# Kernel optimization log

Measured on AMD Instinct MI355X. Metric: run time of the kernel, lower is better.

The kernel has to match this reference:

```python
import jax, jax.numpy as jnp
import numpy as np

B, N, D, S, ITERS = 64, 4096, 256, 8, 3
EPS = 1e-5


def _ln(x, g, b):
    m = jnp.mean(x, axis=-1, keepdims=True)
    v = jnp.mean((x - m) ** 2, axis=-1, keepdims=True)
    return (x - m) * jax.lax.rsqrt(v + EPS) * g + b


def setup_inputs() -> dict:
    key = jax.random.key(0)
    ks = jax.random.split(key, 20)
    s = 1.0 / np.sqrt(D)
    inp = {
        'x': jax.random.normal(ks[0], (B, N, D), jnp.float32),
        'noise': jax.random.normal(ks[1], (B, S, D), jnp.float32),
        'slot_mu': jax.random.normal(ks[2], (1, 1, D), jnp.float32),
        'slot_sigma': jax.random.normal(ks[3], (1, 1, D), jnp.float32) * 0.1,
        'Wq': jax.random.uniform(ks[4], (D, D), jnp.float32, -s, s),
        'bq': jnp.zeros((D,), jnp.float32),
        'Wk': jax.random.uniform(ks[5], (D, D), jnp.float32, -s, s),
        'bk': jnp.zeros((D,), jnp.float32),
        'Wv': jax.random.uniform(ks[6], (D, D), jnp.float32, -s, s),
        'bv': jnp.zeros((D,), jnp.float32),
        'W_ih': jax.random.uniform(ks[7], (3 * D, D), jnp.float32, -s, s),
        'b_ih': jnp.zeros((3 * D,), jnp.float32),
        'W_hh': jax.random.uniform(ks[8], (3 * D, D), jnp.float32, -s, s),
        'b_hh': jnp.zeros((3 * D,), jnp.float32),
        'W1': jax.random.uniform(ks[9], (D, D), jnp.float32, -s, s),
        'b1': jnp.zeros((D,), jnp.float32),
        'W2': jax.random.uniform(ks[10], (D, D), jnp.float32, -s, s),
        'b2': jnp.zeros((D,), jnp.float32),
        'g_in': jnp.ones((D,), jnp.float32), 'be_in': jnp.zeros((D,), jnp.float32),
        'g_sl': jnp.ones((D,), jnp.float32), 'be_sl': jnp.zeros((D,), jnp.float32),
        'g_mlp': jnp.ones((D,), jnp.float32), 'be_mlp': jnp.zeros((D,), jnp.float32),
    }
    return inp


def reference(x, noise, slot_mu, slot_sigma, Wq, bq, Wk, bk, Wv, bv,
              W_ih, b_ih, W_hh, b_hh, W1, b1, W2, b2,
              g_in, be_in, g_sl, be_sl, g_mlp, be_mlp):
    # slot init: mu + exp(sigma) * noise, broadcast over (B, S, D)
    slots = slot_mu + jnp.exp(slot_sigma) * noise

    xn = _ln(x, g_in, be_in)
    k = jnp.einsum('bnd,ed->bne', xn, Wk) + bk
    v = jnp.einsum('bnd,ed->bne', xn, Wv) + bv

    for _ in range(ITERS):
        sn = _ln(slots, g_sl, be_sl)
        q = jnp.einsum('bsd,ed->bse', sn, Wq) + bq
        attn_logits = jnp.einsum('bsd,bnd->bsn', q, k)
        attn = jax.nn.softmax(attn_logits, axis=-1)  # softmax over inputs N (as in source)
        updates = jnp.einsum('bnd,bsn->bsd', v, attn)

        # GRUCell: input=updates, hidden=slots (flattened over B*S)
        u = updates.reshape(-1, D)
        h = slots.reshape(-1, D)
        gx = u @ W_ih.T + b_ih
        gh = h @ W_hh.T + b_hh
        xr, xz, xn_g = jnp.split(gx, 3, axis=-1)
        hr, hz, hn_g = jnp.split(gh, 3, axis=-1)
        r = jax.nn.sigmoid(xr + hr)
        z = jax.nn.sigmoid(xz + hz)
        n = jnp.tanh(xn_g + r * hn_g)
        h = (1.0 - z) * n + z * h
        slots = h.reshape(x.shape[0], -1, D)

        m = _ln(slots, g_mlp, be_mlp)
        slots = slots + jax.nn.relu(m @ W1.T + b1) @ W2.T + b2
    return slots
```

## Files before the change

kernel.cpp:

```cpp
#include <hip/hip_runtime.h>

#define B_ 64
#define N_ 4096
#define D_ 256
#define S_ 8
#define EPSL 1e-5f

typedef _Float16 f16x8 __attribute__((ext_vector_type(8)));
typedef _Float16 f16x4 __attribute__((ext_vector_type(4)));
typedef float f32x4 __attribute__((ext_vector_type(4)));

__device__ __forceinline__ void gload_lds16_nt(const void* g, void* l){
    __builtin_amdgcn_global_load_lds(
        (const __attribute__((address_space(1))) unsigned int*)g,
        (__attribute__((address_space(3))) unsigned int*)l, 16, 0, 2);
}

__global__ __launch_bounds__(256) void k_ln_x(const float* __restrict__ x,
        const float* __restrict__ g, const float* __restrict__ be,
        _Float16* __restrict__ xn) {
    int w = threadIdx.x >> 6, l = threadIdx.x & 63;
    long row = (long)blockIdx.x * 4 + w;
    float4 xv = *(const float4*)(x + row * D_ + l * 4);
    float s = xv.x + xv.y + xv.z + xv.w;
    float q = xv.x*xv.x + xv.y*xv.y + xv.z*xv.z + xv.w*xv.w;
    #pragma unroll
    for (int m = 1; m < 64; m <<= 1) { s += __shfl_xor(s, m); q += __shfl_xor(q, m); }
    float mean = s * (1.0f/D_);
    float var = q * (1.0f/D_) - mean*mean;
    float inv = rsqrtf(var + EPSL);
    float4 gv = *(const float4*)(g + l*4);
    float4 bv = *(const float4*)(be + l*4);
    f16x4 o;
    o[0] = (_Float16)((xv.x-mean)*inv*gv.x + bv.x);
    o[1] = (_Float16)((xv.y-mean)*inv*gv.y + bv.y);
    o[2] = (_Float16)((xv.z-mean)*inv*gv.z + bv.z);
    o[3] = (_Float16)((xv.w-mean)*inv*gv.w + bv.w);
    *(f16x4*)(xn + row * D_ + l*4) = o;
}

__global__ __launch_bounds__(256) void k_wprep(const float* __restrict__ Whh,
        const float* __restrict__ W1, const float* __restrict__ W2,
        _Float16* __restrict__ Whhf, _Float16* __restrict__ W1f,
        _Float16* __restrict__ W2f) {
    int r = blockIdx.x, t = threadIdx.x;
    const float* src; _Float16* dst; int row;
    if (r < 768){ src = Whh; dst = Whhf; row = r; }
    else if (r < 1024){ src = W1; dst = W1f; row = r - 768; }
    else { src = W2; dst = W2f; row = r - 1024; }
    float v = src[(long)(r < 768 ? r : (r < 1024 ? r-768 : r-1024))*256 + t];
    long di = (long)((((row>>4)*8 + (t>>5))*64 + ((t>>3)&3)*16 + (row&15)))*8 + (t&7);
    dst[di] = (_Float16)v;
}

__global__ __launch_bounds__(256) void k_wprep2(const float* __restrict__ Wih,
        const float* __restrict__ Wv, const float* __restrict__ Wq,
        const float* __restrict__ Wk, const float* __restrict__ bih,
        const float* __restrict__ bv, const float* __restrict__ bq,
        _Float16* __restrict__ Wcf, _Float16* __restrict__ Wqkf,
        float* __restrict__ bc, float* __restrict__ cq) {
    __shared__ float a[4][256];
    int r = blockIdx.x, t = threadIdx.x;
    int w = t>>6, l = t&63;
    bool isC = (r < 192);
    if (isC){
        #pragma unroll
        for (int k=0;k<4;k++) a[k][t] = Wih[(long)(r*4+k)*256 + t];
    } else {
        int dbase = (r-192)*4;
        #pragma unroll
        for (int k=0;k<4;k++) a[k][t] = Wk[(long)t*256 + dbase + k];
    }
    __syncthreads();
    float ac[4] = {0.f,0.f,0.f,0.f};
    const float* Bm = isC ? Wv : Wq;
    for (int e=0;e<256;e++){
        float bvv = Bm[(long)e*256 + t];
        ac[0] += a[0][e]*bvv; ac[1] += a[1][e]*bvv;
        ac[2] += a[2][e]*bvv; ac[3] += a[3][e]*bvv;
    }
    _Float16* dst = isC ? Wcf : Wqkf;
    int rb = isC ? r*4 : (r-192)*4;
    #pragma unroll
    for (int k=0;k<4;k++){
        int row = rb + k;
        long di = (long)((((row>>4)*8 + (t>>5))*64 + ((t>>3)&3)*16 + (row&15)))*8 + (t&7);
        dst[di] = (_Float16)ac[k];
    }
    if (w < 4){
        const float* bvec = isC ? bv : bq;
        float p = 0.f;
        #pragma unroll
        for (int q=0;q<4;q++) p += a[w][l + q*64] * bvec[l + q*64];
        #pragma unroll
        for (int m=1;m<64;m<<=1) p += __shfl_xor(p, m);
        if (l==0){
            if (isC) bc[r*4 + w] = p + bih[r*4 + w];
            else     cq[(r-192)*4 + w] = p;
        }
    }
}

__device__ __forceinline__ void a16_st4(_Float16* a, int row, int col, float4 v){
    int byte = row*512 + ((col*2) ^ ((row&7)<<4));
    f16x4 h; h[0]=(_Float16)v.x; h[1]=(_Float16)v.y; h[2]=(_Float16)v.z; h[3]=(_Float16)v.w;
    *(f16x4*)((char*)a + byte) = h;
}
__device__ __forceinline__ void a16_st2(_Float16* a, int row, int col, _Float16 v){
    int byte = row*512 + ((col*2) ^ ((row&7)<<4));
    *(_Float16*)((char*)a + byte) = v;
}
__device__ __forceinline__ f16x8 a16_ld8(const _Float16* a, int row, int col){
    int byte = row*512 + ((col*2) ^ ((row&7)<<4));
    return *(const f16x8*)((const char*)a + byte);
}
__device__ __forceinline__ f16x8 wfrag_ld(const _Float16* __restrict__ Wf,
        int tt, int ks, int l){
    return *(const f16x8*)(Wf + ((long)tt*4096 + (ks*64 + l)*8));
}

template<int NT, int OS>
__device__ __forceinline__ void mm_stage_f(const _Float16* a16,
        const _Float16* __restrict__ Wf, float* outl, int w, int l){
    int lr = l&15, lh = l>>4;
    f16x8 A[8];
    #pragma unroll
    for (int ks=0;ks<8;ks++) A[ks] = a16_ld8(a16, lr, lh*8 + ks*32);
    #pragma unroll
    for (int tile=0; tile<NT; ++tile){
        int tt = w*NT + tile;
        f32x4 acc = {0.f,0.f,0.f,0.f};
        #pragma unroll
        for (int ks=0;ks<8;ks++)
            acc = __builtin_amdgcn_mfma_f32_16x16x32_f16(A[ks], wfrag_ld(Wf,tt,ks,l), acc, 0,0,0);
        if (lh < 2){
            #pragma unroll
            for (int r=0;r<4;r++) outl[(lh*4+r)*OS + tt*16 + lr] = acc[r];
        }
    }
}

__device__ __forceinline__ void mm_gates_f(const _Float16* au, const _Float16* ah,
        const _Float16* __restrict__ Wcf, const _Float16* __restrict__ Whf,
        float* g1, float* g2, int w, int l){
    int lr = l&15, lh = l>>4;
    f16x8 Au[8], Ah[8];
    #pragma unroll
    for (int ks=0;ks<8;ks++){ Au[ks] = a16_ld8(au, lr, lh*8+ks*32);
                              Ah[ks] = a16_ld8(ah, lr, lh*8+ks*32); }
    #pragma unroll
    for (int tile=0; tile<6; ++tile){
        int tt = w*6 + tile;
        f32x4 a1 = {0.f,0.f,0.f,0.f}, a2 = {0.f,0.f,0.f,0.f};
        #pragma unroll
        for (int ks=0;ks<8;ks++)
            a1 = __builtin_amdgcn_mfma_f32_16x16x32_f16(Au[ks], wfrag_ld(Wcf,tt,ks,l), a1, 0,0,0);
        #pragma unroll
        for (int ks=0;ks<8;ks++)
            a2 = __builtin_amdgcn_mfma_f32_16x16x32_f16(Ah[ks], wfrag_ld(Whf,tt,ks,l), a2, 0,0,0);
        if (lh < 2){
            #pragma unroll
            for (int r=0;r<4;r++){
                int s = lh*4+r;
                g1[s*768 + tt*16 + lr] = a1[r];
                g2[s*768 + tt*16 + lr] = a2[r];
            }
        }
    }
}

__global__ __launch_bounds__(512) void k_init(const float* __restrict__ noise,
        const float* __restrict__ mu, const float* __restrict__ sg,
        const float* __restrict__ g_sl, const float* __restrict__ be_sl,
        const _Float16* __restrict__ Wqkf, const float* __restrict__ cq,
        float* __restrict__ slots, _Float16* __restrict__ qh16) {
    __shared__ __align__(16) _Float16 a16[16*256];
    __shared__ float g1[8*256];
    int t = threadIdx.x, w = t>>6, l = t&63, b = blockIdx.x;
    int col = l*4;
    float4 nz = *(const float4*)(noise + ((long)b*8+w)*256 + col);
    float4 muv = *(const float4*)(mu + col);
    float4 sgv = *(const float4*)(sg + col);
    float4 sl;
    sl.x = muv.x + __expf(sgv.x)*nz.x; sl.y = muv.y + __expf(sgv.y)*nz.y;
    sl.z = muv.z + __expf(sgv.z)*nz.z; sl.w = muv.w + __expf(sgv.w)*nz.w;
    *(float4*)(slots + ((long)b*8+w)*256 + col) = sl;
    float s1 = sl.x+sl.y+sl.z+sl.w;
    float s2 = sl.x*sl.x+sl.y*sl.y+sl.z*sl.z+sl.w*sl.w;
    #pragma unroll
    for (int m=1;m<64;m<<=1){ s1+=__shfl_xor(s1,m); s2+=__shfl_xor(s2,m); }
    float mean = s1*(1.0f/D_);
    float inv = rsqrtf(s2*(1.0f/D_) - mean*mean + EPSL);
    float4 gv = *(const float4*)(g_sl + col);
    float4 bb = *(const float4*)(be_sl + col);
    float4 sn;
    sn.x=(sl.x-mean)*inv*gv.x+bb.x; sn.y=(sl.y-mean)*inv*gv.y+bb.y;
    sn.z=(sl.z-mean)*inv*gv.z+bb.z; sn.w=(sl.w-mean)*inv*gv.w+bb.w;
    a16_st4(a16, w, col, sn);
    float4 z = {0.f,0.f,0.f,0.f};
    a16_st4(a16, 8+w, col, z);
    __syncthreads();
    mm_stage_f<2,256>(a16, Wqkf, g1, w, l);
    __syncthreads();
    for (int idx=t; idx<2048; idx+=512){
        int s = idx>>8, d = idx&255;
        qh16[((long)b*16+s)*D_ + d] = (_Float16)(g1[s*256+d] + cq[d]);
        qh16[((long)b*16+8+s)*D_ + d] = (_Float16)0.f;
    }
}

__global__ __launch_bounds__(256) void k_attn(const _Float16* __restrict__ xn,
        const _Float16* __restrict__ qh16,
        _Float16* __restrict__ pacc, float* __restrict__ ppsum,
        float* __restrict__ pmax) {
    __shared__ __align__(16) char xt_raw[4*16384];
    __shared__ __align__(16) float pt_s[4][16][8];
    __shared__ float mw_s[4][8], psw_s[4][8];
    int t = threadIdx.x, w = t>>6, l = t&63, lr = l&15, lh = l>>4;
    int c = blockIdx.x, b = blockIdx.y;

    f16x8 A[8];
    const _Float16* qbase = qh16 + ((long)b*16 + lr)*D_ + lh*8;
    #pragma unroll
    for (int ks=0;ks<8;ks++) A[ks] = *(const f16x8*)(qbase + ks*32);
    asm volatile("s_waitcnt vmcnt(0)" ::: "memory");

    char* xw = xt_raw + w*16384;
    const char* xnb = (const char*)(xn + (long)b*N_*D_);
    int rlo = l>>5;
    int cb  = (l&31)*16;

    {
        int n0 = c*512 + w*16;
        #pragma unroll
        for (int j=0;j<8;j++){
            int row = 2*j + rlo;
            const char* gp = xnb + (long)(n0+row)*512 + (cb ^ ((row&7)<<4));
            gload_lds16_nt(gp, xw + j*1024);
        }
    }

    float m8[8];
    #pragma unroll
    for (int s=0;s<8;s++) m8[s] = -1e30f;
    float acc[8][4] = {};
    float psr[4] = {0.f,0.f,0.f,0.f};
    float (*pt)[8] = pt_s[w];
    int fx = (lr&7)<<4;

    for (int sc=0; sc<8; ++sc){
        const char* curb = xw + ((sc&1)<<13);
        char* nxtb = xw + (((sc+1)&1)<<13);
        if (sc < 7){
            asm volatile("s_waitcnt lgkmcnt(0)" ::: "memory");
            int n0n = c*512 + (sc+1)*64 + w*16;
            #pragma unroll
            for (int j=0;j<8;j++){
                int row = 2*j + rlo;
                const char* gp = xnb + (long)(n0n+row)*512 + (cb ^ ((row&7)<<4));
                gload_lds16_nt(gp, nxtb + j*1024);
            }
            asm volatile("s_waitcnt vmcnt(8)" ::: "memory");
        } else {
            asm volatile("s_waitcnt vmcnt(0)" ::: "memory");
        }
        __builtin_amdgcn_sched_barrier(0);

        f32x4 lacc = {0.f,0.f,0.f,0.f};
        #pragma unroll
        for (int ks=0;ks<8;ks++){
            f16x8 Bf = *(const f16x8*)(curb + lr*512 + ((lh*16 + ks*64) ^ fx));
            lacc = __builtin_amdgcn_mfma_f32_16x16x32_f16(A[ks], Bf, lacc, 0,0,0);
        }
        float tm[4];
        #pragma unroll
        for (int r=0;r<4;r++) tm[r] = lacc[r];
        #pragma unroll
        for (int m=1;m<16;m<<=1){
            #pragma unroll
            for (int r=0;r<4;r++) tm[r] = fmaxf(tm[r], __shfl_xor(tm[r], m));
        }
        float mN[8];
        #pragma unroll
        for (int r=0;r<4;r++){ mN[r] = __shfl(tm[r], lr); mN[4+r] = __shfl(tm[r], 16+lr); }
        float sc8[8];
        #pragma unroll
        for (int s=0;s<8;s++){
            float mn = fmaxf(m8[s], mN[s]);
            sc8[s] = __expf(m8[s] - mn);
            m8[s] = mn;
        }
        #pragma unroll
        for (int s=0;s<8;s++){
            acc[s][0]*=sc8[s]; acc[s][1]*=sc8[s]; acc[s][2]*=sc8[s]; acc[s][3]*=sc8[s];
        }
        if (lh < 2){
            float4 pv;
            #pragma unroll
            for (int r=0;r<4;r++){
                int s = lh*4+r;
                float p = __expf(lacc[r] - m8[s]);
                psr[r] = psr[r]*sc8[s] + p;
                ((float*)&pv)[r] = p;
            }
            *(float4*)&pt[lr][lh*4] = pv;
        }
        #pragma unroll 4
        for (int i=0;i<16;i++){
            float4 p0 = *(const float4*)&pt[i][0];
            float4 p1 = *(const float4*)&pt[i][4];
            f16x4 xv = *(const f16x4*)(curb + i*512 + ((l*8) ^ ((i&7)<<4)));
            float x0=(float)xv[0], x1=(float)xv[1], x2=(float)xv[2], x3=(float)xv[3];
            acc[0][0]+=p0.x*x0; acc[0][1]+=p0.x*x1; acc[0][2]+=p0.x*x2; acc[0][3]+=p0.x*x3;
            acc[1][0]+=p0.y*x0; acc[1][1]+=p0.y*x1; acc[1][2]+=p0.y*x2; acc[1][3]+=p0.y*x3;
            acc[2][0]+=p0.z*x0; acc[2][1]+=p0.z*x1; acc[2][2]+=p0.z*x2; acc[2][3]+=p0.z*x3;
            acc[3][0]+=p0.w*x0; acc[3][1]+=p0.w*x1; acc[3][2]+=p0.w*x2; acc[3][3]+=p0.w*x3;
            acc[4][0]+=p1.x*x0; acc[4][1]+=p1.x*x1; acc[4][2]+=p1.x*x2; acc[4][3]+=p1.x*x3;
            acc[5][0]+=p1.y*x0; acc[5][1]+=p1.y*x1; acc[5][2]+=p1.y*x2; acc[5][3]+=p1.y*x3;
            acc[6][0]+=p1.z*x0; acc[6][1]+=p1.z*x1; acc[6][2]+=p1.z*x2; acc[6][3]+=p1.z*x3;
            acc[7][0]+=p1.w*x0; acc[7][1]+=p1.w*x1; acc[7][2]+=p1.w*x2; acc[7][3]+=p1.w*x3;
        }
    }
    #pragma unroll
    for (int m=1;m<16;m<<=1){
        #pragma unroll
        for (int r=0;r<4;r++) psr[r] += __shfl_xor(psr[r], m);
    }
    if (l == 0){
        #pragma unroll
        for (int s=0;s<8;s++) mw_s[w][s] = m8[s];
        #pragma unroll
        for (int r=0;r<4;r++) psw_s[w][r] = psr[r];
    }
    if (l == 16){
        #pragma unroll
        for (int r=0;r<4;r++) psw_s[w][4+r] = psr[r];
    }
    __syncthreads();
    float M8[8];
    #pragma unroll
    for (int s=0;s<8;s++)
        M8[s] = fmaxf(fmaxf(mw_s[0][s],mw_s[1][s]), fmaxf(mw_s[2][s],mw_s[3][s]));
    float* accw = (float*)xt_raw;
    #pragma unroll
    for (int s=0;s<8;s++){
        float wsc = __expf(m8[s] - M8[s]);
        float4 v;
        v.x=acc[s][0]*wsc; v.y=acc[s][1]*wsc; v.z=acc[s][2]*wsc; v.w=acc[s][3]*wsc;
        *(float4*)&accw[((w*8+s)<<8) + l*4] = v;
    }
    __syncthreads();
    for (int pair=t; pair<2048; pair+=256){
        int s = pair>>8, d = pair&255;
        float v = accw[(s<<8)+d] + accw[((8+s)<<8)+d] + accw[((16+s)<<8)+d] + accw[((24+s)<<8)+d];
        pacc[(((long)b*8 + c)*8 + s)*D_ + d] = (_Float16)v;
    }
    if (t < 8){
        float ps = 0.f;
        #pragma unroll
        for (int w2=0;w2<4;w2++) ps += __expf(mw_s[w2][t]-M8[t]) * psw_s[w2][t];
        ppsum[((long)b*8+c)*8 + t] = ps;
        pmax [((long)b*8+c)*8 + t] = M8[t];
    }
}

__global__ __launch_bounds__(512) void k_tail(
    const _Float16* __restrict__ pacc, const float* __restrict__ ppsum,
    const float* __restrict__ pmax, const float* __restrict__ slots,
    const _Float16* __restrict__ Wcf, const float* __restrict__ bc,
    const _Float16* __restrict__ Whhf, const float* __restrict__ bhh,
    const _Float16* __restrict__ W1f, const float* __restrict__ b1,
    const _Float16* __restrict__ W2f, const float* __restrict__ b2,
    const float* __restrict__ gm, const float* __restrict__ bem,
    const float* __restrict__ g_sl, const float* __restrict__ be_sl,
    const _Float16* __restrict__ Wqkf, const float* __restrict__ cq,
    float* __restrict__ out, _Float16* __restrict__ qh16, int last) {
    int t = threadIdx.x, w = t>>6, l = t&63;
    int b = blockIdx.x;
    __shared__ float hb[8][256], hn[8][256];
    __shared__ float g1[8*768], g2[8*768];
    __shared__ __align__(16) _Float16 a16a[16*256], a16b[16*256];
    __shared__ float pss[8];
    __shared__ float wcs[8][8];

    if (t < 8){
        float pm[8]; float M = -1e30f;
        #pragma unroll
        for (int c=0;c<8;c++){ pm[c] = pmax[((long)b*8+c)*8+t]; M = fmaxf(M, pm[c]); }
        float ps = 0.f;
        #pragma unroll
        for (int c=0;c<8;c++){
            float wc = __expf(pm[c]-M);
            wcs[t][c] = wc;
            ps += wc*ppsum[((long)b*8+c)*8+t];
        }
        pss[t] = ps;
    }
    __syncthreads();
    for (int idx=t; idx<2048; idx+=512){
        int s = idx>>8, d = idx&255;
        float v = 0.f;
        #pragma unroll
        for (int c=0;c<8;c++) v += wcs[s][c]*(float)pacc[(((long)b*8+c)*8+s)*D_ + d];
        float axv = v / pss[s];
        float hbv = slots[((long)b*8+s)*D_ + d];
        hb[s][d] = hbv;
        a16_st2(a16a, s, d, (_Float16)axv);
        a16_st2(a16b, s, d, (_Float16)hbv);
    }
    {   float4 z = {0.f,0.f,0.f,0.f};
        a16_st4(a16a, 8+w, l*4, z);
        a16_st4(a16b, 8+w, l*4, z);
    }
    __syncthreads();
    mm_gates_f(a16a, a16b, Wcf, Whhf, g1, g2, w, l);
    __syncthreads();
    {
        int d0 = l*4;
        float hn4[4];
        #pragma unroll
        for (int i=0;i<4;i++){
            int d = d0+i;
            float r = 1.f/(1.f+__expf(-(g1[w*768+d]     + bc[d]     + g2[w*768+d]     + bhh[d])));
            float z = 1.f/(1.f+__expf(-(g1[w*768+256+d] + bc[256+d] + g2[w*768+256+d] + bhh[256+d])));
            float gg = g1[w*768+512+d] + bc[512+d] + r*(g2[w*768+512+d] + bhh[512+d]);
            float e2 = __expf(2.f*gg);
            float nn = 1.f - 2.f/(e2+1.f);
            hn4[i] = (1.f-z)*nn + z*hb[w][d];
            hn[w][d] = hn4[i];
        }
        float s1 = hn4[0]+hn4[1]+hn4[2]+hn4[3];
        float s2 = hn4[0]*hn4[0]+hn4[1]*hn4[1]+hn4[2]*hn4[2]+hn4[3]*hn4[3];
        #pragma unroll
        for (int m=1;m<64;m<<=1){ s1+=__shfl_xor(s1,m); s2+=__shfl_xor(s2,m); }
        float mean = s1*(1.0f/D_);
        float inv = rsqrtf(s2*(1.0f/D_) - mean*mean + EPSL);
        float4 gv = *(const float4*)(gm + d0);
        float4 bb = *(const float4*)(bem + d0);
        float4 v;
        v.x=(hn4[0]-mean)*inv*gv.x+bb.x; v.y=(hn4[1]-mean)*inv*gv.y+bb.y;
        v.z=(hn4[2]-mean)*inv*gv.z+bb.z; v.w=(hn4[3]-mean)*inv*gv.w+bb.w;
        a16_st4(a16a, w, d0, v);
    }
    __syncthreads();
    mm_stage_f<2,256>(a16a, W1f, g1, w, l);
    __syncthreads();
    {
        int d0 = l*4;
        float4 v = *(const float4*)&g1[w*256+d0];
        float4 bb = *(const float4*)(b1 + d0);
        v.x=fmaxf(v.x+bb.x,0.f); v.y=fmaxf(v.y+bb.y,0.f);
        v.z=fmaxf(v.z+bb.z,0.f); v.w=fmaxf(v.w+bb.w,0.f);
        a16_st4(a16b, w, d0, v);
    }
    __syncthreads();
    mm_stage_f<2,256>(a16b, W2f, g2, w, l);
    __syncthreads();
    {
        int d0 = l*4;
        float4 bb = *(const float4*)(b2 + d0);
        float4 o4;
        o4.x = hn[w][d0]   + g2[w*256+d0]   + bb.x;
        o4.y = hn[w][d0+1] + g2[w*256+d0+1] + bb.y;
        o4.z = hn[w][d0+2] + g2[w*256+d0+2] + bb.z;
        o4.w = hn[w][d0+3] + g2[w*256+d0+3] + bb.w;
        *(float4*)(out + ((long)b*8+w)*D_ + d0) = o4;
        if (!last){
            float s1 = o4.x+o4.y+o4.z+o4.w;
            float s2 = o4.x*o4.x+o4.y*o4.y+o4.z*o4.z+o4.w*o4.w;
            #pragma unroll
            for (int m=1;m<64;m<<=1){ s1+=__shfl_xor(s1,m); s2+=__shfl_xor(s2,m); }
            float mean = s1*(1.0f/D_);
            float inv = rsqrtf(s2*(1.0f/D_) - mean*mean + EPSL);
            float4 gv = *(const float4*)(g_sl + d0);
            float4 be = *(const float4*)(be_sl + d0);
            float4 v;
            v.x=(o4.x-mean)*inv*gv.x+be.x; v.y=(o4.y-mean)*inv*gv.y+be.y;
            v.z=(o4.z-mean)*inv*gv.z+be.z; v.w=(o4.w-mean)*inv*gv.w+be.w;
            a16_st4(a16a, w, d0, v);
        }
    }
    if (last) return;
    __syncthreads();
    mm_stage_f<2,256>(a16a, Wqkf, g1, w, l);
    __syncthreads();
    for (int idx=t; idx<2048; idx+=512){
        int s = idx>>8, d = idx&255;
        qh16[((long)b*16+s)*D_ + d] = (_Float16)(g1[s*256+d] + cq[d]);
    }
}

extern "C" void kernel_launch(void* const* d_in, const int* in_sizes, int n_in,
                              void* d_out, int out_size, void* d_ws, size_t ws_size,
                              hipStream_t stream) {
    const float* x     = (const float*)d_in[0];
    const float* noise = (const float*)d_in[1];
    const float* mu    = (const float*)d_in[2];
    const float* sg    = (const float*)d_in[3];
    const float* Wq    = (const float*)d_in[4];
    const float* bq    = (const float*)d_in[5];
    const float* Wk    = (const float*)d_in[6];
    const float* Wv    = (const float*)d_in[8];
    const float* bv    = (const float*)d_in[9];
    const float* Wih   = (const float*)d_in[10];
    const float* bih   = (const float*)d_in[11];
    const float* Whh   = (const float*)d_in[12];
    const float* bhh   = (const float*)d_in[13];
    const float* W1    = (const float*)d_in[14];
    const float* b1    = (const float*)d_in[15];
    const float* W2    = (const float*)d_in[16];
    const float* b2    = (const float*)d_in[17];
    const float* g_in  = (const float*)d_in[18];
    const float* be_in = (const float*)d_in[19];
    const float* g_sl  = (const float*)d_in[20];
    const float* be_sl = (const float*)d_in[21];
    const float* g_mlp = (const float*)d_in[22];
    const float* be_mlp= (const float*)d_in[23];

    char* ws = (char*)d_ws;
    _Float16* xn16  = (_Float16*)(ws);
    _Float16* qh16  = (_Float16*)(ws + 134217728);
    float*    slots = (float*)   (ws + 134742016);
    _Float16* pacc  = (_Float16*)(ws + 135266304);
    float*    ppsum = (float*)   (ws + 152043520);
    float*    pmax  = (float*)   (ws + 152059904);
    _Float16* w16f  = (_Float16*)(ws + 152076288);
    float*    bc    = (float*)   (ws + 153255936);
    float*    cq    = (float*)   (ws + 153259008);

    _Float16* Wcf  = w16f;
    _Float16* Whhf = w16f + 196608;
    _Float16* W1f  = w16f + 393216;
    _Float16* W2f  = w16f + 458752;
    _Float16* Wqkf = w16f + 524288;

    hipLaunchKernelGGL(k_wprep, dim3(1280), dim3(256), 0, stream,
                       Whh, W1, W2, Whhf, W1f, W2f);
    hipLaunchKernelGGL(k_wprep2, dim3(256), dim3(256), 0, stream,
                       Wih, Wv, Wq, Wk, bih, bv, bq, Wcf, Wqkf, bc, cq);
    hipLaunchKernelGGL(k_ln_x, dim3(65536), dim3(256), 0, stream, x, g_in, be_in, xn16);
    hipLaunchKernelGGL(k_init, dim3(64), dim3(512), 0, stream,
                       noise, mu, sg, g_sl, be_sl, Wqkf, cq, slots, qh16);
    for (int it = 0; it < 3; it++){
        hipLaunchKernelGGL(k_attn, dim3(8,64), dim3(256), 0, stream,
                           xn16, qh16, pacc, ppsum, pmax);
        float* dst = (it==2) ? (float*)d_out : slots;
        hipLaunchKernelGGL(k_tail, dim3(64), dim3(512), 0, stream,
                           pacc, ppsum, pmax, slots,
                           Wcf, bc, Whhf, bhh, W1f, b1, W2f, b2,
                           g_mlp, be_mlp, g_sl, be_sl, Wqkf, cq,
                           dst, qh16, (it==2) ? 1 : 0);
    }
}
```

Baseline: 265.0 us.

## Fuse prep kernels into one launch and attention with tail via last-block counter

Merges the LayerNorm, weight-prep and slot-init kernels into a single k_pre launch. The slot init now computes q directly with scalar fp32 dot products instead of MFMA on the precomputed Wqk. The attention and GRU/MLP tail kernels are fused: the last of the eight chunk blocks per batch, found with an atomic counter, runs the tail. Intermediate gate and MLP buffers are kept in fp16 shared memory, which cuts launches and shared memory but adds fence and atomic overhead, extra rounding, and a serial tail on one 256-thread block.

New measurement: 549.4 us. 107% more time.

```diff
diff --git a/kernel.cpp b/kernel.cpp
--- a/kernel.cpp
+++ b/kernel.cpp
@@ -16,91 +16,6 @@
         (__attribute__((address_space(3))) unsigned int*)l, 16, 0, 2);
 }
 
-__global__ __launch_bounds__(256) void k_ln_x(const float* __restrict__ x,
-        const float* __restrict__ g, const float* __restrict__ be,
-        _Float16* __restrict__ xn) {
-    int w = threadIdx.x >> 6, l = threadIdx.x & 63;
-    long row = (long)blockIdx.x * 4 + w;
-    float4 xv = *(const float4*)(x + row * D_ + l * 4);
-    float s = xv.x + xv.y + xv.z + xv.w;
-    float q = xv.x*xv.x + xv.y*xv.y + xv.z*xv.z + xv.w*xv.w;
-    #pragma unroll
-    for (int m = 1; m < 64; m <<= 1) { s += __shfl_xor(s, m); q += __shfl_xor(q, m); }
-    float mean = s * (1.0f/D_);
-    float var = q * (1.0f/D_) - mean*mean;
-    float inv = rsqrtf(var + EPSL);
-    float4 gv = *(const float4*)(g + l*4);
-    float4 bv = *(const float4*)(be + l*4);
-    f16x4 o;
-    o[0] = (_Float16)((xv.x-mean)*inv*gv.x + bv.x);
-    o[1] = (_Float16)((xv.y-mean)*inv*gv.y + bv.y);
-    o[2] = (_Float16)((xv.z-mean)*inv*gv.z + bv.z);
-    o[3] = (_Float16)((xv.w-mean)*inv*gv.w + bv.w);
-    *(f16x4*)(xn + row * D_ + l*4) = o;
-}
-
-__global__ __launch_bounds__(256) void k_wprep(const float* __restrict__ Whh,
-        const float* __restrict__ W1, const float* __restrict__ W2,
-        _Float16* __restrict__ Whhf, _Float16* __restrict__ W1f,
-        _Float16* __restrict__ W2f) {
-    int r = blockIdx.x, t = threadIdx.x;
-    const float* src; _Float16* dst; int row;
-    if (r < 768){ src = Whh; dst = Whhf; row = r; }
-    else if (r < 1024){ src = W1; dst = W1f; row = r - 768; }
-    else { src = W2; dst = W2f; row = r - 1024; }
-    float v = src[(long)(r < 768 ? r : (r < 1024 ? r-768 : r-1024))*256 + t];
-    long di = (long)((((row>>4)*8 + (t>>5))*64 + ((t>>3)&3)*16 + (row&15)))*8 + (t&7);
-    dst[di] = (_Float16)v;
-}
-
-__global__ __launch_bounds__(256) void k_wprep2(const float* __restrict__ Wih,
-        const float* __restrict__ Wv, const float* __restrict__ Wq,
-        const float* __restrict__ Wk, const float* __restrict__ bih,
-        const float* __restrict__ bv, const float* __restrict__ bq,
-        _Float16* __restrict__ Wcf, _Float16* __restrict__ Wqkf,
-        float* __restrict__ bc, float* __restrict__ cq) {
-    __shared__ float a[4][256];
-    int r = blockIdx.x, t = threadIdx.x;
-    int w = t>>6, l = t&63;
-    bool isC = (r < 192);
-    if (isC){
-        #pragma unroll
-        for (int k=0;k<4;k++) a[k][t] = Wih[(long)(r*4+k)*256 + t];
-    } else {
-        int dbase = (r-192)*4;
-        #pragma unroll
-        for (int k=0;k<4;k++) a[k][t] = Wk[(long)t*256 + dbase + k];
-    }
-    __syncthreads();
-    float ac[4] = {0.f,0.f,0.f,0.f};
-    const float* Bm = isC ? Wv : Wq;
-    for (int e=0;e<256;e++){
-        float bvv = Bm[(long)e*256 + t];
-        ac[0] += a[0][e]*bvv; ac[1] += a[1][e]*bvv;
-        ac[2] += a[2][e]*bvv; ac[3] += a[3][e]*bvv;
-    }
-    _Float16* dst = isC ? Wcf : Wqkf;
-    int rb = isC ? r*4 : (r-192)*4;
-    #pragma unroll
-    for (int k=0;k<4;k++){
-        int row = rb + k;
-        long di = (long)((((row>>4)*8 + (t>>5))*64 + ((t>>3)&3)*16 + (row&15)))*8 + (t&7);
-        dst[di] = (_Float16)ac[k];
-    }
-    if (w < 4){
-        const float* bvec = isC ? bv : bq;
-        float p = 0.f;
-        #pragma unroll
-        for (int q=0;q<4;q++) p += a[w][l + q*64] * bvec[l + q*64];
-        #pragma unroll
-        for (int m=1;m<64;m<<=1) p += __shfl_xor(p, m);
-        if (l==0){
-            if (isC) bc[r*4 + w] = p + bih[r*4 + w];
-            else     cq[(r-192)*4 + w] = p;
-        }
-    }
-}
-
 __device__ __forceinline__ void a16_st4(_Float16* a, int row, int col, float4 v){
     int byte = row*512 + ((col*2) ^ ((row&7)<<4));
     f16x4 h; h[0]=(_Float16)v.x; h[1]=(_Float16)v.y; h[2]=(_Float16)v.z; h[3]=(_Float16)v.w;
@@ -119,38 +34,163 @@
     return *(const f16x8*)(Wf + ((long)tt*4096 + (ks*64 + l)*8));
 }
 
-template<int NT, int OS>
-__device__ __forceinline__ void mm_stage_f(const _Float16* a16,
-        const _Float16* __restrict__ Wf, float* outl, int w, int l){
+__global__ __launch_bounds__(256) void k_pre(
+        const float* __restrict__ x, const float* __restrict__ g_in,
+        const float* __restrict__ be_in, _Float16* __restrict__ xn,
+        const float* __restrict__ Whh, const float* __restrict__ W1,
+        const float* __restrict__ W2, _Float16* __restrict__ Whhf,
+        _Float16* __restrict__ W1f, _Float16* __restrict__ W2f,
+        const float* __restrict__ Wih, const float* __restrict__ Wv,
+        const float* __restrict__ Wq, const float* __restrict__ Wk,
+        const float* __restrict__ bih, const float* __restrict__ bv,
+        const float* __restrict__ bq, _Float16* __restrict__ Wcf,
+        _Float16* __restrict__ Wqkf, float* __restrict__ bc,
+        float* __restrict__ cq,
+        const float* __restrict__ noise, const float* __restrict__ mu,
+        const float* __restrict__ sg, const float* __restrict__ g_sl,
+        const float* __restrict__ be_sl, float* __restrict__ slots,
+        _Float16* __restrict__ qh16, unsigned* __restrict__ cnt) {
+    __shared__ float a4[4][256];
+    __shared__ float sn[256], ql[256], red[10];
+    int r = blockIdx.x, t = threadIdx.x;
+    int w = t>>6, l = t&63;
+    if (r < 65536){
+        long row = (long)r * 4 + w;
+        float4 xv = *(const float4*)(x + row * D_ + l * 4);
+        float s = xv.x + xv.y + xv.z + xv.w;
+        float q = xv.x*xv.x + xv.y*xv.y + xv.z*xv.z + xv.w*xv.w;
+        #pragma unroll
+        for (int m = 1; m < 64; m <<= 1) { s += __shfl_xor(s, m); q += __shfl_xor(q, m); }
+        float mean = s * (1.0f/D_);
+        float inv = rsqrtf(q * (1.0f/D_) - mean*mean + EPSL);
+        float4 gv = *(const float4*)(g_in + l*4);
+        float4 bb = *(const float4*)(be_in + l*4);
+        f16x4 o;
+        o[0] = (_Float16)((xv.x-mean)*inv*gv.x + bb.x);
+        o[1] = (_Float16)((xv.y-mean)*inv*gv.y + bb.y);
+        o[2] = (_Float16)((xv.z-mean)*inv*gv.z + bb.z);
+        o[3] = (_Float16)((xv.w-mean)*inv*gv.w + bb.w);
+        *(f16x4*)(xn + row * D_ + l*4) = o;
+        return;
+    }
+    if (r < 66816){
+        int rr = r - 65536;
+        const float* src; _Float16* dst; int row;
+        if (rr < 768){ src = Whh; dst = Whhf; row = rr; }
+        else if (rr < 1024){ src = W1; dst = W1f; row = rr - 768; }
+        else { src = W2; dst = W2f; row = rr - 1024; }
+        float v = src[(long)row*256 + t];
+        long di = (long)((((row>>4)*8 + (t>>5))*64 + ((t>>3)&3)*16 + (row&15)))*8 + (t&7);
+        dst[di] = (_Float16)v;
+        return;
+    }
+    if (r < 67072){
+        int rr = r - 66816;
+        bool isC = (rr < 192);
+        if (isC){
+            #pragma unroll
+            for (int k=0;k<4;k++) a4[k][t] = Wih[(long)(rr*4+k)*256 + t];
+        } else {
+            int dbase = (rr-192)*4;
+            #pragma unroll
+            for (int k=0;k<4;k++) a4[k][t] = Wk[(long)t*256 + dbase + k];
+        }
+        __syncthreads();
+        float ac[4] = {0.f,0.f,0.f,0.f};
+        const float* Bm = isC ? Wv : Wq;
+        for (int e=0;e<256;e++){
+            float bvv = Bm[(long)e*256 + t];
+            ac[0] += a4[0][e]*bvv; ac[1] += a4[1][e]*bvv;
+            ac[2] += a4[2][e]*bvv; ac[3] += a4[3][e]*bvv;
+        }
+        _Float16* dst = isC ? Wcf : Wqkf;
+        int rb = isC ? rr*4 : (rr-192)*4;
+        #pragma unroll
+        for (int k=0;k<4;k++){
+            int row = rb + k;
+            long di = (long)((((row>>4)*8 + (t>>5))*64 + ((t>>3)&3)*16 + (row&15)))*8 + (t&7);
+            dst[di] = (_Float16)ac[k];
+        }
+        if (w < 4){
+            const float* bvec = isC ? bv : bq;
+            float p = 0.f;
+            #pragma unroll
+            for (int q=0;q<4;q++) p += a4[w][l + q*64] * bvec[l + q*64];
+            #pragma unroll
+            for (int m=1;m<64;m<<=1) p += __shfl_xor(p, m);
+            if (l==0){
+                if (isC) bc[rr*4 + w] = p + bih[rr*4 + w];
+                else     cq[(rr-192)*4 + w] = p;
+            }
+        }
+        return;
+    }
+    {
+        int rr = r - 67072;
+        int b = rr>>3, s8 = rr&7;
+        long base = (long)(b*8+s8) * D_;
+        float v = mu[t] + __expf(sg[t]) * noise[base + t];
+        slots[base + t] = v;
+        float s = v, q = v*v;
+        #pragma unroll
+        for (int m=1;m<64;m<<=1){ s+=__shfl_xor(s,m); q+=__shfl_xor(q,m);}
+        if (l==0){ red[w]=s; red[4+w]=q; }
+        __syncthreads();
+        if (t==0){
+            float ss=red[0]+red[1]+red[2]+red[3];
+            float qq=red[4]+red[5]+red[6]+red[7];
+            float mean = ss*(1.0f/D_);
+            red[8]=mean; red[9]=rsqrtf(qq*(1.0f/D_) - mean*mean + EPSL);
+            if (s8 == 0) cnt[b] = 0u;
+        }
+        __syncthreads();
+        float mean=red[8], inv=red[9];
+        sn[t] = (v-mean)*inv*g_sl[t] + be_sl[t];
+        __syncthreads();
+        float acc = bq[t];
+        const float4* wr = (const float4*)(Wq + (long)t*D_);
+        const float4* sv = (const float4*)sn;
+        for (int e=0;e<64;e++){ float4 a=wr[e], b4=sv[e];
+            acc += a.x*b4.x + a.y*b4.y + a.z*b4.z + a.w*b4.w; }
+        ql[t]=acc;
+        __syncthreads();
+        float qh=0.f;
+        for (int e=0;e<D_;e++) qh += ql[e]*Wk[(long)e*D_ + t];
+        qh16[((long)b*16 + s8)*D_ + t] = (_Float16)qh;
+        qh16[((long)b*16 + 8 + s8)*D_ + t] = (_Float16)0.f;
+    }
+}
+
+__device__ __forceinline__ void mm_stage4(const _Float16* a16,
+        const _Float16* __restrict__ Wf, _Float16* outl, int w, int l){
     int lr = l&15, lh = l>>4;
     f16x8 A[8];
     #pragma unroll
     for (int ks=0;ks<8;ks++) A[ks] = a16_ld8(a16, lr, lh*8 + ks*32);
     #pragma unroll
-    for (int tile=0; tile<NT; ++tile){
-        int tt = w*NT + tile;
+    for (int tile=0; tile<4; ++tile){
+        int tt = w*4 + tile;
         f32x4 acc = {0.f,0.f,0.f,0.f};
         #pragma unroll
         for (int ks=0;ks<8;ks++)
             acc = __builtin_amdgcn_mfma_f32_16x16x32_f16(A[ks], wfrag_ld(Wf,tt,ks,l), acc, 0,0,0);
         if (lh < 2){
             #pragma unroll
-            for (int r=0;r<4;r++) outl[(lh*4+r)*OS + tt*16 + lr] = acc[r];
-        }
-    }
-}
-
-__device__ __forceinline__ void mm_gates_f(const _Float16* au, const _Float16* ah,
+            for (int r=0;r<4;r++) outl[(lh*4+r)*256 + tt*16 + lr] = (_Float16)acc[r];
+        }
+    }
+}
+__device__ __forceinline__ void mm_gates4(const _Float16* au, const _Float16* ah,
         const _Float16* __restrict__ Wcf, const _Float16* __restrict__ Whf,
-        float* g1, float* g2, int w, int l){
+        _Float16* g1, _Float16* g2, int w, int l){
     int lr = l&15, lh = l>>4;
     f16x8 Au[8], Ah[8];
     #pragma unroll
     for (int ks=0;ks<8;ks++){ Au[ks] = a16_ld8(au, lr, lh*8+ks*32);
                               Ah[ks] = a16_ld8(ah, lr, lh*8+ks*32); }
     #pragma unroll
-    for (int tile=0; tile<6; ++tile){
-        int tt = w*6 + tile;
+    for (int tile=0; tile<12; ++tile){
+        int tt = w*12 + tile;
         f32x4 a1 = {0.f,0.f,0.f,0.f}, a2 = {0.f,0.f,0.f,0.f};
         #pragma unroll
         for (int ks=0;ks<8;ks++)
@@ -162,76 +202,46 @@
             #pragma unroll
             for (int r=0;r<4;r++){
                 int s = lh*4+r;
-                g1[s*768 + tt*16 + lr] = a1[r];
-                g2[s*768 + tt*16 + lr] = a2[r];
+                g1[s*768 + tt*16 + lr] = (_Float16)a1[r];
+                g2[s*768 + tt*16 + lr] = (_Float16)a2[r];
             }
         }
     }
 }
 
-__global__ __launch_bounds__(512) void k_init(const float* __restrict__ noise,
-        const float* __restrict__ mu, const float* __restrict__ sg,
+__global__ __launch_bounds__(256) void k_attntail(const _Float16* __restrict__ xn,
+        _Float16* __restrict__ qh16, _Float16* __restrict__ pacc,
+        float* __restrict__ ppsum, float* __restrict__ pmax,
+        float* __restrict__ slots,
+        const _Float16* __restrict__ Wcf, const float* __restrict__ bc,
+        const _Float16* __restrict__ Whhf, const float* __restrict__ bhh,
+        const _Float16* __restrict__ W1f, const float* __restrict__ b1,
+        const _Float16* __restrict__ W2f, const float* __restrict__ b2,
+        const float* __restrict__ gm, const float* __restrict__ bem,
         const float* __restrict__ g_sl, const float* __restrict__ be_sl,
         const _Float16* __restrict__ Wqkf, const float* __restrict__ cq,
-        float* __restrict__ slots, _Float16* __restrict__ qh16) {
-    __shared__ __align__(16) _Float16 a16[16*256];
-    __shared__ float g1[8*256];
-    int t = threadIdx.x, w = t>>6, l = t&63, b = blockIdx.x;
-    int col = l*4;
-    float4 nz = *(const float4*)(noise + ((long)b*8+w)*256 + col);
-    float4 muv = *(const float4*)(mu + col);
-    float4 sgv = *(const float4*)(sg + col);
-    float4 sl;
-    sl.x = muv.x + __expf(sgv.x)*nz.x; sl.y = muv.y + __expf(sgv.y)*nz.y;
-    sl.z = muv.z + __expf(sgv.z)*nz.z; sl.w = muv.w + __expf(sgv.w)*nz.w;
-    *(float4*)(slots + ((long)b*8+w)*256 + col) = sl;
-    float s1 = sl.x+sl.y+sl.z+sl.w;
-    float s2 = sl.x*sl.x+sl.y*sl.y+sl.z*sl.z+sl.w*sl.w;
-    #pragma unroll
-    for (int m=1;m<64;m<<=1){ s1+=__shfl_xor(s1,m); s2+=__shfl_xor(s2,m); }
-    float mean = s1*(1.0f/D_);
-    float inv = rsqrtf(s2*(1.0f/D_) - mean*mean + EPSL);
-    float4 gv = *(const float4*)(g_sl + col);
-    float4 bb = *(const float4*)(be_sl + col);
-    float4 sn;
-    sn.x=(sl.x-mean)*inv*gv.x+bb.x; sn.y=(sl.y-mean)*inv*gv.y+bb.y;
-    sn.z=(sl.z-mean)*inv*gv.z+bb.z; sn.w=(sl.w-mean)*inv*gv.w+bb.w;
-    a16_st4(a16, w, col, sn);
-    float4 z = {0.f,0.f,0.f,0.f};
-    a16_st4(a16, 8+w, col, z);
-    __syncthreads();
-    mm_stage_f<2,256>(a16, Wqkf, g1, w, l);
-    __syncthreads();
-    for (int idx=t; idx<2048; idx+=512){
-        int s = idx>>8, d = idx&255;
-        qh16[((long)b*16+s)*D_ + d] = (_Float16)(g1[s*256+d] + cq[d]);
-        qh16[((long)b*16+8+s)*D_ + d] = (_Float16)0.f;
-    }
-}
-
-__global__ __launch_bounds__(256) void k_attn(const _Float16* __restrict__ xn,
-        const _Float16* __restrict__ qh16,
-        _Float16* __restrict__ pacc, float* __restrict__ ppsum,
-        float* __restrict__ pmax) {
-    __shared__ __align__(16) char xt_raw[4*16384];
-    __shared__ __align__(16) float pt_s[4][16][8];
-    __shared__ float mw_s[4][8], psw_s[4][8];
+        float* __restrict__ out, unsigned* __restrict__ cnt, int it, int last) {
+    __shared__ __align__(16) char smem[67840];
+    __shared__ unsigned lastflag;
     int t = threadIdx.x, w = t>>6, l = t&63, lr = l&15, lh = l>>4;
     int c = blockIdx.x, b = blockIdx.y;
 
+    float (*pt_s)[16][8] = (float (*)[16][8])(smem + 65536);
+    float (*mw_s)[8]  = (float (*)[8])(smem + 67584);
+    float (*psw_s)[8] = (float (*)[8])(smem + 67712);
+
     f16x8 A[8];
     const _Float16* qbase = qh16 + ((long)b*16 + lr)*D_ + lh*8;
     #pragma unroll
     for (int ks=0;ks<8;ks++) A[ks] = *(const f16x8*)(qbase + ks*32);
     asm volatile("s_waitcnt vmcnt(0)" ::: "memory");
 
-    char* xw = xt_raw + w*16384;
+    char* xw = smem + w*16384;
     const char* xnb = (const char*)(xn + (long)b*N_*D_);
     int rlo = l>>5;
     int cb  = (l&31)*16;
 
-    {
-        int n0 = c*512 + w*16;
+    {   int n0 = c*512 + w*16;
         #pragma unroll
         for (int j=0;j<8;j++){
             int row = 2*j + rlo;
@@ -341,7 +351,7 @@
     #pragma unroll
     for (int s=0;s<8;s++)
         M8[s] = fmaxf(fmaxf(mw_s[0][s],mw_s[1][s]), fmaxf(mw_s[2][s],mw_s[3][s]));
-    float* accw = (float*)xt_raw;
+    float* accw = (float*)smem;
     #pragma unroll
     for (int s=0;s<8;s++){
         float wsc = __expf(m8[s] - M8[s]);
@@ -362,72 +372,73 @@
         ppsum[((long)b*8+c)*8 + t] = ps;
         pmax [((long)b*8+c)*8 + t] = M8[t];
     }
-}
-
-__global__ __launch_bounds__(512) void k_tail(
-    const _Float16* __restrict__ pacc, const float* __restrict__ ppsum,
-    const float* __restrict__ pmax, const float* __restrict__ slots,
-    const _Float16* __restrict__ Wcf, const float* __restrict__ bc,
-    const _Float16* __restrict__ Whhf, const float* __restrict__ bhh,
-    const _Float16* __restrict__ W1f, const float* __restrict__ b1,
-    const _Float16* __restrict__ W2f, const float* __restrict__ b2,
-    const float* __restrict__ gm, const float* __restrict__ bem,
-    const float* __restrict__ g_sl, const float* __restrict__ be_sl,
-    const _Float16* __restrict__ Wqkf, const float* __restrict__ cq,
-    float* __restrict__ out, _Float16* __restrict__ qh16, int last) {
-    int t = threadIdx.x, w = t>>6, l = t&63;
-    int b = blockIdx.x;
-    __shared__ float hb[8][256], hn[8][256];
-    __shared__ float g1[8*768], g2[8*768];
-    __shared__ __align__(16) _Float16 a16a[16*256], a16b[16*256];
-    __shared__ float pss[8];
-    __shared__ float wcs[8][8];
+    __threadfence();
+    __syncthreads();
+    if (t == 0){
+        unsigned old = atomicAdd(&cnt[b], 1u);
+        lastflag = (old == (unsigned)(it*8 + 7)) ? 1u : 0u;
+    }
+    __syncthreads();
+    if (!lastflag) return;
+    __threadfence();
+
+    float*     hbp  = (float*)smem;
+    float*     hnp  = (float*)(smem + 8192);
+    _Float16*  g1h  = (_Float16*)(smem + 16384);
+    _Float16*  g2h  = (_Float16*)(smem + 28672);
+    _Float16*  a16a = (_Float16*)(smem + 40960);
+    _Float16*  a16b = (_Float16*)(smem + 49152);
+    float*     wcs  = (float*)(smem + 57344);
+    float*     pss  = (float*)(smem + 57600);
 
     if (t < 8){
         float pm[8]; float M = -1e30f;
         #pragma unroll
-        for (int c=0;c<8;c++){ pm[c] = pmax[((long)b*8+c)*8+t]; M = fmaxf(M, pm[c]); }
+        for (int cc=0;cc<8;cc++){ pm[cc] = pmax[((long)b*8+cc)*8+t]; M = fmaxf(M, pm[cc]); }
         float ps = 0.f;
         #pragma unroll
-        for (int c=0;c<8;c++){
-            float wc = __expf(pm[c]-M);
-            wcs[t][c] = wc;
-            ps += wc*ppsum[((long)b*8+c)*8+t];
+        for (int cc=0;cc<8;cc++){
+            float wc = __expf(pm[cc]-M);
+            wcs[t*8+cc] = wc;
+            ps += wc*ppsum[((long)b*8+cc)*8+t];
         }
         pss[t] = ps;
     }
     __syncthreads();
-    for (int idx=t; idx<2048; idx+=512){
+    for (int idx=t; idx<2048; idx+=256){
         int s = idx>>8, d = idx&255;
         float v = 0.f;
         #pragma unroll
-        for (int c=0;c<8;c++) v += wcs[s][c]*(float)pacc[(((long)b*8+c)*8+s)*D_ + d];
+        for (int cc=0;cc<8;cc++) v += wcs[s*8+cc]*(float)pacc[(((long)b*8+cc)*8+s)*D_ + d];
         float axv = v / pss[s];
         float hbv = slots[((long)b*8+s)*D_ + d];
-        hb[s][d] = hbv;
+        hbp[s*256+d] = hbv;
         a16_st2(a16a, s, d, (_Float16)axv);
         a16_st2(a16b, s, d, (_Float16)hbv);
     }
     {   float4 z = {0.f,0.f,0.f,0.f};
-        a16_st4(a16a, 8+w, l*4, z);
-        a16_st4(a16b, 8+w, l*4, z);
-    }
-    __syncthreads();
-    mm_gates_f(a16a, a16b, Wcf, Whhf, g1, g2, w, l);
-    __syncthreads();
-    {
+        a16_st4(a16a, 8+w, l*4, z);  a16_st4(a16a, 12+w, l*4, z);
+        a16_st4(a16b, 8+w, l*4, z);  a16_st4(a16b, 12+w, l*4, z);
+    }
+    __syncthreads();
+    mm_gates4(a16a, a16b, Wcf, Whhf, g1h, g2h, w, l);
+    __syncthreads();
+    for (int rr = w; rr < 8; rr += 4){
         int d0 = l*4;
         float hn4[4];
         #pragma unroll
         for (int i=0;i<4;i++){
             int d = d0+i;
-            float r = 1.f/(1.f+__expf(-(g1[w*768+d]     + bc[d]     + g2[w*768+d]     + bhh[d])));
-            float z = 1.f/(1.f+__expf(-(g1[w*768+256+d] + bc[256+d] + g2[w*768+256+d] + bhh[256+d])));
-            float gg = g1[w*768+512+d] + bc[512+d] + r*(g2[w*768+512+d] + bhh[512+d]);
+            float xr=(float)g1h[rr*768+d],     hr=(float)g2h[rr*768+d];
+            float xz=(float)g1h[rr*768+256+d], hz=(float)g2h[rr*768+256+d];
+            float xg=(float)g1h[rr*768+512+d], hg=(float)g2h[rr*768+512+d];
+            float rg = 1.f/(1.f+__expf(-(xr + bc[d]     + hr + bhh[d])));
+            float zg = 1.f/(1.f+__expf(-(xz + bc[256+d] + hz + bhh[256+d])));
+            float gg = xg + bc[512+d] + rg*(hg + bhh[512+d]);
             float e2 = __expf(2.f*gg);
             float nn = 1.f - 2.f/(e2+1.f);
-            hn4[i] = (1.f-z)*nn + z*hb[w][d];
-            hn[w][d] = hn4[i];
+            hn4[i] = (1.f-zg)*nn + zg*hbp[rr*256+d];
+            hnp[rr*256+d] = hn4[i];
         }
         float s1 = hn4[0]+hn4[1]+hn4[2]+hn4[3];
         float s2 = hn4[0]*hn4[0]+hn4[1]*hn4[1]+hn4[2]*hn4[2]+hn4[3]*hn4[3];
@@ -440,31 +451,33 @@
         float4 v;
         v.x=(hn4[0]-mean)*inv*gv.x+bb.x; v.y=(hn4[1]-mean)*inv*gv.y+bb.y;
         v.z=(hn4[2]-mean)*inv*gv.z+bb.z; v.w=(hn4[3]-mean)*inv*gv.w+bb.w;
-        a16_st4(a16a, w, d0, v);
-    }
-    __syncthreads();
-    mm_stage_f<2,256>(a16a, W1f, g1, w, l);
-    __syncthreads();
-    {
+        a16_st4(a16a, rr, d0, v);
+    }
+    __syncthreads();
+    mm_stage4(a16a, W1f, g1h, w, l);
+    __syncthreads();
+    for (int rr = w; rr < 8; rr += 4){
         int d0 = l*4;
-        float4 v = *(const float4*)&g1[w*256+d0];
         float4 bb = *(const float4*)(b1 + d0);
-        v.x=fmaxf(v.x+bb.x,0.f); v.y=fmaxf(v.y+bb.y,0.f);
-        v.z=fmaxf(v.z+bb.z,0.f); v.w=fmaxf(v.w+bb.w,0.f);
-        a16_st4(a16b, w, d0, v);
-    }
-    __syncthreads();
-    mm_stage_f<2,256>(a16b, W2f, g2, w, l);
-    __syncthreads();
-    {
+        float4 v;
+        v.x=fmaxf((float)g1h[rr*256+d0]  +bb.x,0.f);
+        v.y=fmaxf((float)g1h[rr*256+d0+1]+bb.y,0.f);
+        v.z=fmaxf((float)g1h[rr*256+d0+2]+bb.z,0.f);
+        v.w=fmaxf((float)g1h[rr*256+d0+3]+bb.w,0.f);
+        a16_st4(a16b, rr, d0, v);
+    }
+    __syncthreads();
+    mm_stage4(a16b, W2f, g2h, w, l);
+    __syncthreads();
+    for (int rr = w; rr < 8; rr += 4){
         int d0 = l*4;
         float4 bb = *(const float4*)(b2 + d0);
         float4 o4;
-        o4.x = hn[w][d0]   + g2[w*256+d0]   + bb.x;
-        o4.y = hn[w][d0+1] + g2[w*256+d0+1] + bb.y;
-        o4.z = hn[w][d0+2] + g2[w*256+d0+2] + bb.z;
-        o4.w = hn[w][d0+3] + g2[w*256+d0+3] + bb.w;
-        *(float4*)(out + ((long)b*8+w)*D_ + d0) = o4;
+        o4.x = hnp[rr*256+d0]   + (float)g2h[rr*256+d0]   + bb.x;
+        o4.y = hnp[rr*256+d0+1] + (float)g2h[rr*256+d0+1] + bb.y;
+        o4.z = hnp[rr*256+d0+2] + (float)g2h[rr*256+d0+2] + bb.z;
+        o4.w = hnp[rr*256+d0+3] + (float)g2h[rr*256+d0+3] + bb.w;
+        *(float4*)(out + ((long)b*8+rr)*D_ + d0) = o4;
         if (!last){
             float s1 = o4.x+o4.y+o4.z+o4.w;
             float s2 = o4.x*o4.x+o4.y*o4.y+o4.z*o4.z+o4.w*o4.w;
@@ -477,16 +490,16 @@
             float4 v;
             v.x=(o4.x-mean)*inv*gv.x+be.x; v.y=(o4.y-mean)*inv*gv.y+be.y;
             v.z=(o4.z-mean)*inv*gv.z+be.z; v.w=(o4.w-mean)*inv*gv.w+be.w;
-            a16_st4(a16a, w, d0, v);
+            a16_st4(a16a, rr, d0, v);
         }
     }
     if (last) return;
     __syncthreads();
-    mm_stage_f<2,256>(a16a, Wqkf, g1, w, l);
-    __syncthreads();
-    for (int idx=t; idx<2048; idx+=512){
+    mm_stage4(a16a, Wqkf, g1h, w, l);
+    __syncthreads();
+    for (int idx=t; idx<2048; idx+=256){
         int s = idx>>8, d = idx&255;
-        qh16[((long)b*16+s)*D_ + d] = (_Float16)(g1[s*256+d] + cq[d]);
+        qh16[((long)b*16+s)*D_ + d] = (_Float16)((float)g1h[s*256+d] + cq[d]);
     }
 }
 
@@ -527,6 +540,7 @@
     _Float16* w16f  = (_Float16*)(ws + 152076288);
     float*    bc    = (float*)   (ws + 153255936);
     float*    cq    = (float*)   (ws + 153259008);
+    unsigned* cnt   = (unsigned*)(ws + 153260032);
 
     _Float16* Wcf  = w16f;
     _Float16* Whhf = w16f + 196608;
@@ -534,21 +548,17 @@
     _Float16* W2f  = w16f + 458752;
     _Float16* Wqkf = w16f + 524288;
 
-    hipLaunchKernelGGL(k_wprep, dim3(1280), dim3(256), 0, stream,
-                       Whh, W1, W2, Whhf, W1f, W2f);
-    hipLaunchKernelGGL(k_wprep2, dim3(256), dim3(256), 0, stream,
-                       Wih, Wv, Wq, Wk, bih, bv, bq, Wcf, Wqkf, bc, cq);
-    hipLaunchKernelGGL(k_ln_x, dim3(65536), dim3(256), 0, stream, x, g_in, be_in, xn16);
-    hipLaunchKernelGGL(k_init, dim3(64), dim3(512), 0, stream,
-                       noise, mu, sg, g_sl, be_sl, Wqkf, cq, slots, qh16);
+    hipLaunchKernelGGL(k_pre, dim3(67584), dim3(256), 0, stream,
+                       x, g_in, be_in, xn16,
+                       Whh, W1, W2, Whhf, W1f, W2f,
+                       Wih, Wv, Wq, Wk, bih, bv, bq, Wcf, Wqkf, bc, cq,
+                       noise, mu, sg, g_sl, be_sl, slots, qh16, cnt);
     for (int it = 0; it < 3; it++){
-        hipLaunchKernelGGL(k_attn, dim3(8,64), dim3(256), 0, stream,
-                           xn16, qh16, pacc, ppsum, pmax);
         float* dst = (it==2) ? (float*)d_out : slots;
-        hipLaunchKernelGGL(k_tail, dim3(64), dim3(512), 0, stream,
-                           pacc, ppsum, pmax, slots,
+        hipLaunchKernelGGL(k_attntail, dim3(8,64), dim3(256), 0, stream,
+                           xn16, qh16, pacc, ppsum, pmax, slots,
                            Wcf, bc, Whhf, bhh, W1f, b1, W2f, b2,
                            g_mlp, be_mlp, g_sl, be_sl, Wqkf, cq,
-                           dst, qh16, (it==2) ? 1 : 0);
-    }
-}
+                           dst, cnt, it, (it==2) ? 1 : 0);
+    }
+}
```
